# Performance work log

Hardware: AMD Instinct MI355X
Metric: run time of the kernel (lower is better)

## Reference

```python
import jax, jax.numpy as jnp
import numpy as np

N_WIRES = 8
DIM = 1 << N_WIRES  # 256

# --- static precompute: CNOT-ring basis permutation and PauliZ sign matrix ---
# torchquantum convention: wire 0 is the most significant bit of the basis index.
_gates = [(w, w + 1) for w in range(N_WIRES - 1)] + [(N_WIRES - 1, 0)]
_perm = np.empty(DIM, dtype=np.int64)
for b in range(DIM):
    bits = [(b >> (N_WIRES - 1 - w)) & 1 for w in range(N_WIRES)]
    for c, t in _gates:
        if bits[c]:
            bits[t] ^= 1
    _perm[b] = sum(bit << (N_WIRES - 1 - w) for w, bit in enumerate(bits))
_Z = np.array([[1.0 - 2.0 * ((idx >> (N_WIRES - 1 - w)) & 1) for w in range(N_WIRES)]
               for idx in range(DIM)], dtype=np.float32)
# exp_Z[w] = sum_b probs_in[b] * Z[perm[b], w]  (CNOTs permute basis states)
_M = jnp.asarray(_Z[_perm])  # [256, 8]


def _quantum_head(angles):
    """angles: [..., 8] RX angles -> PauliZ expectations [..., 8].

    Circuit: RX(angle_w) on each wire from |0>, CNOT ring, MeasureAll(PauliZ).
    Post-RX state is a product state; CNOTs only permute basis states, so
    probabilities suffice (no complex amplitudes needed).
    """
    half = angles * 0.5
    c2 = jnp.cos(half) ** 2  # P(qubit=0)
    s2 = jnp.sin(half) ** 2  # P(qubit=1)
    # Build the 256-dim joint probability vector via sequential outer products.
    p = jnp.ones(angles.shape[:-1] + (1,), angles.dtype)
    for w in range(N_WIRES):
        pw = jnp.stack([c2[..., w], s2[..., w]], axis=-1)  # [..., 2]
        p = (p[..., :, None] * pw[..., None, :]).reshape(angles.shape[:-1] + (-1,))
    return p @ _M.astype(p.dtype)  # [..., 8]


def setup_inputs() -> dict:
    key = jax.random.key(0)
    ks = jax.random.split(key, 6)
    B, S, E = 8, 512, 768
    scale = 1.0 / np.sqrt(E)
    return {
        "x": jax.random.normal(ks[0], (B, S, E), jnp.float32),
        "W_proj": jax.random.normal(ks[1], (E, E), jnp.float32) * scale,
        "b_proj": jax.random.normal(ks[2], (E,), jnp.float32) * 0.02,
        "theta": jax.random.normal(ks[3], (N_WIRES,), jnp.float32),
        "W_comb": jax.random.normal(ks[4], (E, E), jnp.float32) * scale,
        "b_comb": jax.random.normal(ks[5], (E,), jnp.float32) * 0.02,
    }


def reference(x, W_proj, b_proj, theta, W_comb, b_comb):
    B, S, E = x.shape
    H = E // N_WIRES  # num_heads = 96
    proj = x @ W_proj.T + b_proj                 # [B, S, E] (torch Linear)
    angles = proj.reshape(B, S, H, N_WIRES) + theta  # encoder RX(x) then RX(theta): angles add
    expz = _quantum_head(angles)                 # [B, S, H, 8]
    out = expz.reshape(B, S, E)                  # heads re-concatenated
    # dropout is identity in eval mode
    return out @ W_comb.T + b_comb
```

## Files before the change

kernel.cpp:

```cpp
#include <hip/hip_runtime.h>

typedef _Float16 v8h __attribute__((ext_vector_type(8)));
typedef float    v4f __attribute__((ext_vector_type(4)));

__device__ __forceinline__ void gl_lds16(const void* g, void* l) {
  __builtin_amdgcn_global_load_lds(
      (__attribute__((address_space(1))) void*)(void*)g,
      (__attribute__((address_space(3))) void*)l, 16, 0, 0);
}
__device__ __forceinline__ v8h cvt8(const float4 a, const float4 b) {
  v8h o;
  o[0] = (_Float16)a.x; o[1] = (_Float16)a.y; o[2] = (_Float16)a.z; o[3] = (_Float16)a.w;
  o[4] = (_Float16)b.x; o[5] = (_Float16)b.y; o[6] = (_Float16)b.z; o[7] = (_Float16)b.w;
  return o;
}

__global__ void conv_w(const float4* __restrict__ wp, const float4* __restrict__ wc,
                       v8h* __restrict__ op, v8h* __restrict__ oc) {
  const int n = 73728;
  int i = blockIdx.x * blockDim.x + threadIdx.x;
  const float4* src = (i < n) ? wp : wc;
  v8h* dst = (i < n) ? op : oc;
  const int j = (i < n) ? i : i - n;
  dst[j] = cvt8(src[2 * j], src[2 * j + 1]);
}


__global__ __launch_bounds__(256) void gemm1_qh(
    const float* __restrict__ X,
    const _Float16* __restrict__ B,
    const float* __restrict__ bp,
    const float* __restrict__ theta,
    _Float16* __restrict__ EZ) {
  const int t = threadIdx.x;
  const int b = blockIdx.x;
  const int xcd = b & 7, slot = b >> 3;
  const int bm = xcd * 8 + slot / 12;
  const int bn = slot % 12;

  const int wave = t >> 6, lane = t & 63;
  const int quad = lane >> 4, l16 = lane & 15;
  const int wm = (wave >> 1) * 32, wn = (wave & 1) * 32;

  __shared__ __align__(16) unsigned char smem[32768];
  float* Cs = (float*)smem;

  const float4 th0 = *(const float4*)theta;
  const float4 th1 = *(const float4*)(theta + 4);

  const int r = t >> 3;
  const int cg = t & 7;
  const int lcg = cg ^ (r & 7);

  const float*    Xg = X + (size_t)(bm * 64 + r) * 768 + lcg * 8;
  const _Float16* Bg = B + (size_t)(bn * 64 + r) * 768 + lcg * 8;

  v4f acc[2][2];
#pragma unroll
  for (int i = 0; i < 2; i++)
#pragma unroll
    for (int j = 0; j < 2; j++) acc[i][j] = (v4f){0.f, 0.f, 0.f, 0.f};

  float4 xr[4];
#pragma unroll
  for (int c = 0; c < 2; c++) {
    const float* p = Xg + (size_t)c * 32 * 768;
    xr[2 * c]     = *(const float4*)p;
    xr[2 * c + 1] = *(const float4*)(p + 4);
  }
  {
    _Float16* B0 = (_Float16*)(smem + 16384);
    gl_lds16(Bg, &B0[t * 8]);
    gl_lds16(Bg + (size_t)32 * 768, &B0[2048 + t * 8]);
    _Float16* A0 = (_Float16*)smem;
    *(v8h*)&A0[t * 8]        = cvt8(xr[0], xr[1]);
    *(v8h*)&A0[2048 + t * 8] = cvt8(xr[2], xr[3]);
  }
#pragma unroll
  for (int c = 0; c < 2; c++) {
    const float* p = Xg + (size_t)c * 32 * 768 + 64;
    xr[2 * c]     = *(const float4*)p;
    xr[2 * c + 1] = *(const float4*)(p + 4);
  }
  __syncthreads();

#pragma unroll
  for (int it = 0; it < 12; ++it) {
    _Float16* Ac = (_Float16*)(smem + (it & 1) * 8192);
    _Float16* Bc = (_Float16*)(smem + 16384 + (it & 1) * 8192);
    if (it < 11) {
      _Float16* An = (_Float16*)(smem + ((it + 1) & 1) * 8192);
      _Float16* Bn = (_Float16*)(smem + 16384 + ((it + 1) & 1) * 8192);
      const int kn = (it + 1) * 64;
      gl_lds16(Bg + kn, &Bn[t * 8]);
      gl_lds16(Bg + (size_t)32 * 768 + kn, &Bn[2048 + t * 8]);
      *(v8h*)&An[t * 8]        = cvt8(xr[0], xr[1]);
      *(v8h*)&An[2048 + t * 8] = cvt8(xr[2], xr[3]);
      if (it < 10) {
        const int kf = (it + 2) * 64;
#pragma unroll
        for (int c = 0; c < 2; c++) {
          const float* p = Xg + (size_t)c * 32 * 768 + kf;
          xr[2 * c]     = *(const float4*)p;
          xr[2 * c + 1] = *(const float4*)(p + 4);
        }
      }
    }
#pragma unroll
    for (int q = 0; q < 2; q++) {
      v8h af[2], bf[2];
#pragma unroll
      for (int i = 0; i < 2; i++)
        af[i] = *(const v8h*)&Ac[(wm + i * 16 + l16) * 64 + ((((q << 2) + quad) ^ (l16 & 7)) << 3)];
#pragma unroll
      for (int j = 0; j < 2; j++)
        bf[j] = *(const v8h*)&Bc[(wn + j * 16 + l16) * 64 + ((((q << 2) + quad) ^ (l16 & 7)) << 3)];
#pragma unroll
      for (int i = 0; i < 2; i++)
#pragma unroll
        for (int j = 0; j < 2; j++)
          acc[i][j] = __builtin_amdgcn_mfma_f32_16x16x32_f16(af[i], bf[j], acc[i][j], 0, 0, 0);
    }
    __syncthreads();
  }

  const int r0 = wm + quad * 4;
  const int c0 = wn + l16;
#pragma unroll
  for (int j = 0; j < 2; j++)
#pragma unroll
    for (int i = 0; i < 2; i++)
#pragma unroll
      for (int rr = 0; rr < 4; rr++)
        Cs[(r0 + i * 16 + rr) * 68 + c0 + j * 16] = acc[i][j][rr];
  __syncthreads();

#pragma unroll
  for (int s = 0; s < 2; s++) {
    const int idx = t + s * 256;
    const int row = idx >> 3, h = idx & 7;
    const int gcol = bn * 64 + h * 8;
    const float* cr = &Cs[row * 68 + h * 8];
    const float4 q0 = *(const float4*)cr;
    const float4 q1 = *(const float4*)(cr + 4);
    const float4 b0 = *(const float4*)(bp + gcol);
    const float4 b1 = *(const float4*)(bp + gcol + 4);
    float c[8];
    c[0] = cosf(q0.x + b0.x + th0.x);
    c[1] = cosf(q0.y + b0.y + th0.y);
    c[2] = cosf(q0.z + b0.z + th0.z);
    c[3] = cosf(q0.w + b0.w + th0.w);
    c[4] = cosf(q1.x + b1.x + th1.x);
    c[5] = cosf(q1.y + b1.y + th1.y);
    c[6] = cosf(q1.z + b1.z + th1.z);
    c[7] = cosf(q1.w + b1.w + th1.w);
    float e[8];
    e[0] = c[1] * c[2] * c[3] * c[4] * c[5] * c[6] * c[7];
    float pr = c[0];
#pragma unroll
    for (int w = 1; w < 8; w++) { pr *= c[w]; e[w] = pr; }
    v8h ov;
#pragma unroll
    for (int w = 0; w < 8; w++) ov[w] = (_Float16)e[w];
    *(v8h*)(EZ + (size_t)(bm * 64 + row) * 768 + gcol) = ov;
  }
}

__global__ __launch_bounds__(256) void gemm2(
    const _Float16* __restrict__ A,
    const _Float16* __restrict__ B,
    float* __restrict__ C,
    const float* __restrict__ bias) {
  const int t = threadIdx.x;
  const int b = blockIdx.x;
  const int xcd = b & 7, slot = b >> 3;
  const int bm = xcd * 8 + slot / 12;
  const int bn = slot % 12;

  const int wave = t >> 6, lane = t & 63;
  const int quad = lane >> 4, l16 = lane & 15;
  const int wm = (wave >> 1) * 32, wn = (wave & 1) * 32;

  __shared__ __align__(16) unsigned char smem[32768];

  const int r = t >> 3;
  const int cg = t & 7;
  const int lcg = cg ^ (r & 7);

  const _Float16* Ag = A + (size_t)(bm * 64 + r) * 768 + lcg * 8;
  const _Float16* Bg = B + (size_t)(bn * 64 + r) * 768 + lcg * 8;

  v4f acc[2][2];
#pragma unroll
  for (int i = 0; i < 2; i++)
#pragma unroll
    for (int j = 0; j < 2; j++) acc[i][j] = (v4f){0.f, 0.f, 0.f, 0.f};

  {
    _Float16* A0 = (_Float16*)smem;
    _Float16* B0 = (_Float16*)(smem + 16384);
    gl_lds16(Ag, &A0[t * 8]);
    gl_lds16(Ag + (size_t)32 * 768, &A0[2048 + t * 8]);
    gl_lds16(Bg, &B0[t * 8]);
    gl_lds16(Bg + (size_t)32 * 768, &B0[2048 + t * 8]);
  }
  __syncthreads();

#pragma unroll
  for (int it = 0; it < 12; ++it) {
    _Float16* Ac = (_Float16*)(smem + (it & 1) * 8192);
    _Float16* Bc = (_Float16*)(smem + 16384 + (it & 1) * 8192);
    if (it < 11) {
      _Float16* An = (_Float16*)(smem + ((it + 1) & 1) * 8192);
      _Float16* Bn = (_Float16*)(smem + 16384 + ((it + 1) & 1) * 8192);
      const int kn = (it + 1) * 64;
      gl_lds16(Ag + kn, &An[t * 8]);
      gl_lds16(Ag + (size_t)32 * 768 + kn, &An[2048 + t * 8]);
      gl_lds16(Bg + kn, &Bn[t * 8]);
      gl_lds16(Bg + (size_t)32 * 768 + kn, &Bn[2048 + t * 8]);
    }
#pragma unroll
    for (int q = 0; q < 2; q++) {
      v8h af[2], bf[2];
#pragma unroll
      for (int i = 0; i < 2; i++)
        af[i] = *(const v8h*)&Ac[(wm + i * 16 + l16) * 64 + ((((q << 2) + quad) ^ (l16 & 7)) << 3)];
#pragma unroll
      for (int j = 0; j < 2; j++)
        bf[j] = *(const v8h*)&Bc[(wn + j * 16 + l16) * 64 + ((((q << 2) + quad) ^ (l16 & 7)) << 3)];
#pragma unroll
      for (int ii = 0; ii < 2; ii++)
#pragma unroll
        for (int j = 0; j < 2; j++)
          acc[ii][j] = __builtin_amdgcn_mfma_f32_16x16x32_f16(af[ii], bf[j], acc[ii][j], 0, 0, 0);
    }
    __syncthreads();
  }

  const int row0 = bm * 64 + wm + quad * 4;
  const int col0 = bn * 64 + wn + l16;
#pragma unroll
  for (int j = 0; j < 2; j++) {
    const int col = col0 + j * 16;
    const float bv = bias[col];
#pragma unroll
    for (int i = 0; i < 2; i++) {
#pragma unroll
      for (int rr = 0; rr < 4; rr++) {
        C[(size_t)(row0 + i * 16 + rr) * 768 + col] = acc[i][j][rr] + bv;
      }
    }
  }
}

extern "C" void kernel_launch(void* const* d_in, const int* in_sizes, int n_in,
                              void* d_out, int out_size, void* d_ws, size_t ws_size,
                              hipStream_t stream) {
  const float* x     = (const float*)d_in[0];
  const float* Wp    = (const float*)d_in[1];
  const float* bp    = (const float*)d_in[2];
  const float* theta = (const float*)d_in[3];
  const float* Wcf   = (const float*)d_in[4];
  const float* bc    = (const float*)d_in[5];
  float* out = (float*)d_out;

  const size_t EE = (size_t)768 * 768;

  _Float16* WPH = (_Float16*)d_ws;
  _Float16* WCH = WPH + EE;
  _Float16* EZ  = WCH + EE;

  conv_w<<<(int)(2 * EE / 8 / 256), 256, 0, stream>>>(
      (const float4*)Wp, (const float4*)Wcf, (v8h*)WPH, (v8h*)WCH);

  gemm1_qh<<<768, 256, 0, stream>>>(x, WPH, bp, theta, EZ);

  gemm2<<<768, 256, 0, stream>>>(EZ, WCH, out, bc);
}
```

Baseline: 99.33 us.

## Fuse weight conversion and both GEMMs into one persistent kernel with row flags

Drops the separate weight-conversion kernel and converts fp32 weights to fp16 inline while staging tiles, and merges the two GEMM kernels into one launch. Blocks that share a row tile synchronize through a global atomic counter before running the second GEMM on the EZ rows their siblings produced. This removes two kernel launches and the intermediate fp16 weight buffers. In exchange, every block converts weight tiles redundantly and spins on flags, which relies on all 768 blocks being co-resident (hence launch_bounds with 3 blocks per CU) to avoid deadlock. It also adds a memset launch.

New measurement: 207.1 us. 2.08x slower.

```diff
diff --git a/kernel.cpp b/kernel.cpp
--- a/kernel.cpp
+++ b/kernel.cpp
@@ -15,23 +15,16 @@
   return o;
 }
 
-__global__ void conv_w(const float4* __restrict__ wp, const float4* __restrict__ wc,
-                       v8h* __restrict__ op, v8h* __restrict__ oc) {
-  const int n = 73728;
-  int i = blockIdx.x * blockDim.x + threadIdx.x;
-  const float4* src = (i < n) ? wp : wc;
-  v8h* dst = (i < n) ? op : oc;
-  const int j = (i < n) ? i : i - n;
-  dst[j] = cvt8(src[2 * j], src[2 * j + 1]);
-}
-
-
-__global__ __launch_bounds__(256) void gemm1_qh(
+__global__ __launch_bounds__(256, 3) void fused_all(
     const float* __restrict__ X,
-    const _Float16* __restrict__ B,
+    const float* __restrict__ Wp,
     const float* __restrict__ bp,
     const float* __restrict__ theta,
-    _Float16* __restrict__ EZ) {
+    const float* __restrict__ Wc,
+    const float* __restrict__ bc,
+    float* __restrict__ OUT,
+    _Float16* __restrict__ EZ,
+    int* __restrict__ flags) {
   const int t = threadIdx.x;
   const int b = blockIdx.x;
   const int xcd = b & 7, slot = b >> 3;
@@ -52,202 +45,216 @@
   const int cg = t & 7;
   const int lcg = cg ^ (r & 7);
 
-  const float*    Xg = X + (size_t)(bm * 64 + r) * 768 + lcg * 8;
-  const _Float16* Bg = B + (size_t)(bn * 64 + r) * 768 + lcg * 8;
-
   v4f acc[2][2];
-#pragma unroll
-  for (int i = 0; i < 2; i++)
-#pragma unroll
-    for (int j = 0; j < 2; j++) acc[i][j] = (v4f){0.f, 0.f, 0.f, 0.f};
-
-  float4 xr[4];
-#pragma unroll
-  for (int c = 0; c < 2; c++) {
-    const float* p = Xg + (size_t)c * 32 * 768;
-    xr[2 * c]     = *(const float4*)p;
-    xr[2 * c + 1] = *(const float4*)(p + 4);
+
+  {
+    const float* Xg = X  + (size_t)(bm * 64 + r) * 768 + lcg * 8;
+    const float* Bg = Wp + (size_t)(bn * 64 + r) * 768 + lcg * 8;
+
+#pragma unroll
+    for (int i = 0; i < 2; i++)
+#pragma unroll
+      for (int j = 0; j < 2; j++) acc[i][j] = (v4f){0.f, 0.f, 0.f, 0.f};
+
+    float4 xr[4], br[4];
+#pragma unroll
+    for (int c = 0; c < 2; c++) {
+      const float* px = Xg + (size_t)c * 32 * 768;
+      const float* pb = Bg + (size_t)c * 32 * 768;
+      xr[2 * c] = *(const float4*)px; xr[2 * c + 1] = *(const float4*)(px + 4);
+      br[2 * c] = *(const float4*)pb; br[2 * c + 1] = *(const float4*)(pb + 4);
+    }
+    {
+      _Float16* A0 = (_Float16*)smem;
+      _Float16* B0 = (_Float16*)(smem + 16384);
+      *(v8h*)&A0[t * 8]        = cvt8(xr[0], xr[1]);
+      *(v8h*)&A0[2048 + t * 8] = cvt8(xr[2], xr[3]);
+      *(v8h*)&B0[t * 8]        = cvt8(br[0], br[1]);
+      *(v8h*)&B0[2048 + t * 8] = cvt8(br[2], br[3]);
+    }
+#pragma unroll
+    for (int c = 0; c < 2; c++) {
+      const float* px = Xg + (size_t)c * 32 * 768 + 64;
+      const float* pb = Bg + (size_t)c * 32 * 768 + 64;
+      xr[2 * c] = *(const float4*)px; xr[2 * c + 1] = *(const float4*)(px + 4);
+      br[2 * c] = *(const float4*)pb; br[2 * c + 1] = *(const float4*)(pb + 4);
+    }
+    __syncthreads();
+
+#pragma unroll
+    for (int it = 0; it < 12; ++it) {
+      _Float16* Ac = (_Float16*)(smem + (it & 1) * 8192);
+      _Float16* Bc = (_Float16*)(smem + 16384 + (it & 1) * 8192);
+      if (it < 11) {
+        _Float16* An = (_Float16*)(smem + ((it + 1) & 1) * 8192);
+        _Float16* Bn = (_Float16*)(smem + 16384 + ((it + 1) & 1) * 8192);
+        *(v8h*)&An[t * 8]        = cvt8(xr[0], xr[1]);
+        *(v8h*)&An[2048 + t * 8] = cvt8(xr[2], xr[3]);
+        *(v8h*)&Bn[t * 8]        = cvt8(br[0], br[1]);
+        *(v8h*)&Bn[2048 + t * 8] = cvt8(br[2], br[3]);
+        if (it < 10) {
+          const int kf = (it + 2) * 64;
+#pragma unroll
+          for (int c = 0; c < 2; c++) {
+            const float* px = Xg + (size_t)c * 32 * 768 + kf;
+            const float* pb = Bg + (size_t)c * 32 * 768 + kf;
+            xr[2 * c] = *(const float4*)px; xr[2 * c + 1] = *(const float4*)(px + 4);
+            br[2 * c] = *(const float4*)pb; br[2 * c + 1] = *(const float4*)(pb + 4);
+          }
+        }
+      }
+#pragma unroll
+      for (int q = 0; q < 2; q++) {
+        v8h af[2], bf[2];
+#pragma unroll
+        for (int i = 0; i < 2; i++)
+          af[i] = *(const v8h*)&Ac[(wm + i * 16 + l16) * 64 + ((((q << 2) + quad) ^ (l16 & 7)) << 3)];
+#pragma unroll
+        for (int j = 0; j < 2; j++)
+          bf[j] = *(const v8h*)&Bc[(wn + j * 16 + l16) * 64 + ((((q << 2) + quad) ^ (l16 & 7)) << 3)];
+#pragma unroll
+        for (int i = 0; i < 2; i++)
+#pragma unroll
+          for (int j = 0; j < 2; j++)
+            acc[i][j] = __builtin_amdgcn_mfma_f32_16x16x32_f16(af[i], bf[j], acc[i][j], 0, 0, 0);
+      }
+      __syncthreads();
+    }
+
+    const int r0 = wm + quad * 4;
+    const int c0 = wn + l16;
+#pragma unroll
+    for (int j = 0; j < 2; j++)
+#pragma unroll
+      for (int i = 0; i < 2; i++)
+#pragma unroll
+        for (int rr = 0; rr < 4; rr++)
+          Cs[(r0 + i * 16 + rr) * 68 + c0 + j * 16] = acc[i][j][rr];
+    __syncthreads();
+
+#pragma unroll
+    for (int s = 0; s < 2; s++) {
+      const int idx = t + s * 256;
+      const int row = idx >> 3, h = idx & 7;
+      const int gcol = bn * 64 + h * 8;
+      const float* cr = &Cs[row * 68 + h * 8];
+      const float4 q0 = *(const float4*)cr;
+      const float4 q1 = *(const float4*)(cr + 4);
+      const float4 b0 = *(const float4*)(bp + gcol);
+      const float4 b1 = *(const float4*)(bp + gcol + 4);
+      float c[8];
+      c[0] = cosf(q0.x + b0.x + th0.x);
+      c[1] = cosf(q0.y + b0.y + th0.y);
+      c[2] = cosf(q0.z + b0.z + th0.z);
+      c[3] = cosf(q0.w + b0.w + th0.w);
+      c[4] = cosf(q1.x + b1.x + th1.x);
+      c[5] = cosf(q1.y + b1.y + th1.y);
+      c[6] = cosf(q1.z + b1.z + th1.z);
+      c[7] = cosf(q1.w + b1.w + th1.w);
+      float e[8];
+      e[0] = c[1] * c[2] * c[3] * c[4] * c[5] * c[6] * c[7];
+      float pr = c[0];
+#pragma unroll
+      for (int w = 1; w < 8; w++) { pr *= c[w]; e[w] = pr; }
+      v8h ov;
+#pragma unroll
+      for (int w = 0; w < 8; w++) ov[w] = (_Float16)e[w];
+      *(v8h*)(EZ + (size_t)(bm * 64 + row) * 768 + gcol) = ov;
+    }
   }
-  {
-    _Float16* B0 = (_Float16*)(smem + 16384);
-    gl_lds16(Bg, &B0[t * 8]);
-    gl_lds16(Bg + (size_t)32 * 768, &B0[2048 + t * 8]);
-    _Float16* A0 = (_Float16*)smem;
-    *(v8h*)&A0[t * 8]        = cvt8(xr[0], xr[1]);
-    *(v8h*)&A0[2048 + t * 8] = cvt8(xr[2], xr[3]);
-  }
-#pragma unroll
-  for (int c = 0; c < 2; c++) {
-    const float* p = Xg + (size_t)c * 32 * 768 + 64;
-    xr[2 * c]     = *(const float4*)p;
-    xr[2 * c + 1] = *(const float4*)(p + 4);
+
+  __threadfence();
+  __syncthreads();
+  if (t == 0)
+    __hip_atomic_fetch_add(&flags[bm], 1, __ATOMIC_RELEASE, __HIP_MEMORY_SCOPE_AGENT);
+
+  if (t == 0) {
+    while (__hip_atomic_load(&flags[bm], __ATOMIC_ACQUIRE, __HIP_MEMORY_SCOPE_AGENT) < 12)
+      __builtin_amdgcn_s_sleep(8);
   }
   __syncthreads();
 
-#pragma unroll
-  for (int it = 0; it < 12; ++it) {
-    _Float16* Ac = (_Float16*)(smem + (it & 1) * 8192);
-    _Float16* Bc = (_Float16*)(smem + 16384 + (it & 1) * 8192);
-    if (it < 11) {
-      _Float16* An = (_Float16*)(smem + ((it + 1) & 1) * 8192);
-      _Float16* Bn = (_Float16*)(smem + 16384 + ((it + 1) & 1) * 8192);
-      const int kn = (it + 1) * 64;
-      gl_lds16(Bg + kn, &Bn[t * 8]);
-      gl_lds16(Bg + (size_t)32 * 768 + kn, &Bn[2048 + t * 8]);
-      *(v8h*)&An[t * 8]        = cvt8(xr[0], xr[1]);
-      *(v8h*)&An[2048 + t * 8] = cvt8(xr[2], xr[3]);
-      if (it < 10) {
-        const int kf = (it + 2) * 64;
-#pragma unroll
-        for (int c = 0; c < 2; c++) {
-          const float* p = Xg + (size_t)c * 32 * 768 + kf;
-          xr[2 * c]     = *(const float4*)p;
-          xr[2 * c + 1] = *(const float4*)(p + 4);
+  {
+    const _Float16* Ag = EZ + (size_t)(bm * 64 + r) * 768 + lcg * 8;
+    const float*    Bg = Wc + (size_t)(bn * 64 + r) * 768 + lcg * 8;
+
+#pragma unroll
+    for (int i = 0; i < 2; i++)
+#pragma unroll
+      for (int j = 0; j < 2; j++) acc[i][j] = (v4f){0.f, 0.f, 0.f, 0.f};
+
+    float4 wr[4];
+    {
+      _Float16* A0 = (_Float16*)smem;
+      _Float16* B0 = (_Float16*)(smem + 16384);
+      gl_lds16(Ag, &A0[t * 8]);
+      gl_lds16(Ag + (size_t)32 * 768, &A0[2048 + t * 8]);
+#pragma unroll
+      for (int c = 0; c < 2; c++) {
+        const float* pb = Bg + (size_t)c * 32 * 768;
+        wr[2 * c] = *(const float4*)pb; wr[2 * c + 1] = *(const float4*)(pb + 4);
+      }
+      *(v8h*)&B0[t * 8]        = cvt8(wr[0], wr[1]);
+      *(v8h*)&B0[2048 + t * 8] = cvt8(wr[2], wr[3]);
+    }
+#pragma unroll
+    for (int c = 0; c < 2; c++) {
+      const float* pb = Bg + (size_t)c * 32 * 768 + 64;
+      wr[2 * c] = *(const float4*)pb; wr[2 * c + 1] = *(const float4*)(pb + 4);
+    }
+    __syncthreads();
+
+#pragma unroll
+    for (int it = 0; it < 12; ++it) {
+      _Float16* Ac = (_Float16*)(smem + (it & 1) * 8192);
+      _Float16* Bc = (_Float16*)(smem + 16384 + (it & 1) * 8192);
+      if (it < 11) {
+        _Float16* An = (_Float16*)(smem + ((it + 1) & 1) * 8192);
+        _Float16* Bn = (_Float16*)(smem + 16384 + ((it + 1) & 1) * 8192);
+        const int kn = (it + 1) * 64;
+        gl_lds16(Ag + kn, &An[t * 8]);
+        gl_lds16(Ag + (size_t)32 * 768 + kn, &An[2048 + t * 8]);
+        *(v8h*)&Bn[t * 8]        = cvt8(wr[0], wr[1]);
+        *(v8h*)&Bn[2048 + t * 8] = cvt8(wr[2], wr[3]);
+        if (it < 10) {
+          const int kf = (it + 2) * 64;
+#pragma unroll
+          for (int c = 0; c < 2; c++) {
+            const float* pb = Bg + (size_t)c * 32 * 768 + kf;
+            wr[2 * c] = *(const float4*)pb; wr[2 * c + 1] = *(const float4*)(pb + 4);
+          }
         }
       }
-    }
-#pragma unroll
-    for (int q = 0; q < 2; q++) {
-      v8h af[2], bf[2];
-#pragma unroll
-      for (int i = 0; i < 2; i++)
-        af[i] = *(const v8h*)&Ac[(wm + i * 16 + l16) * 64 + ((((q << 2) + quad) ^ (l16 & 7)) << 3)];
-#pragma unroll
-      for (int j = 0; j < 2; j++)
-        bf[j] = *(const v8h*)&Bc[(wn + j * 16 + l16) * 64 + ((((q << 2) + quad) ^ (l16 & 7)) << 3)];
-#pragma unroll
-      for (int i = 0; i < 2; i++)
+#pragma unroll
+      for (int q = 0; q < 2; q++) {
+        v8h af[2], bf[2];
+#pragma unroll
+        for (int i = 0; i < 2; i++)
+          af[i] = *(const v8h*)&Ac[(wm + i * 16 + l16) * 64 + ((((q << 2) + quad) ^ (l16 & 7)) << 3)];
 #pragma unroll
         for (int j = 0; j < 2; j++)
-          acc[i][j] = __builtin_amdgcn_mfma_f32_16x16x32_f16(af[i], bf[j], acc[i][j], 0, 0, 0);
-    }
-    __syncthreads();
-  }
-
-  const int r0 = wm + quad * 4;
-  const int c0 = wn + l16;
-#pragma unroll
-  for (int j = 0; j < 2; j++)
-#pragma unroll
-    for (int i = 0; i < 2; i++)
-#pragma unroll
-      for (int rr = 0; rr < 4; rr++)
-        Cs[(r0 + i * 16 + rr) * 68 + c0 + j * 16] = acc[i][j][rr];
-  __syncthreads();
-
-#pragma unroll
-  for (int s = 0; s < 2; s++) {
-    const int idx = t + s * 256;
-    const int row = idx >> 3, h = idx & 7;
-    const int gcol = bn * 64 + h * 8;
-    const float* cr = &Cs[row * 68 + h * 8];
-    const float4 q0 = *(const float4*)cr;
-    const float4 q1 = *(const float4*)(cr + 4);
-    const float4 b0 = *(const float4*)(bp + gcol);
-    const float4 b1 = *(const float4*)(bp + gcol + 4);
-    float c[8];
-    c[0] = cosf(q0.x + b0.x + th0.x);
-    c[1] = cosf(q0.y + b0.y + th0.y);
-    c[2] = cosf(q0.z + b0.z + th0.z);
-    c[3] = cosf(q0.w + b0.w + th0.w);
-    c[4] = cosf(q1.x + b1.x + th1.x);
-    c[5] = cosf(q1.y + b1.y + th1.y);
-    c[6] = cosf(q1.z + b1.z + th1.z);
-    c[7] = cosf(q1.w + b1.w + th1.w);
-    float e[8];
-    e[0] = c[1] * c[2] * c[3] * c[4] * c[5] * c[6] * c[7];
-    float pr = c[0];
-#pragma unroll
-    for (int w = 1; w < 8; w++) { pr *= c[w]; e[w] = pr; }
-    v8h ov;
-#pragma unroll
-    for (int w = 0; w < 8; w++) ov[w] = (_Float16)e[w];
-    *(v8h*)(EZ + (size_t)(bm * 64 + row) * 768 + gcol) = ov;
-  }
-}
-
-__global__ __launch_bounds__(256) void gemm2(
-    const _Float16* __restrict__ A,
-    const _Float16* __restrict__ B,
-    float* __restrict__ C,
-    const float* __restrict__ bias) {
-  const int t = threadIdx.x;
-  const int b = blockIdx.x;
-  const int xcd = b & 7, slot = b >> 3;
-  const int bm = xcd * 8 + slot / 12;
-  const int bn = slot % 12;
-
-  const int wave = t >> 6, lane = t & 63;
-  const int quad = lane >> 4, l16 = lane & 15;
-  const int wm = (wave >> 1) * 32, wn = (wave & 1) * 32;
-
-  __shared__ __align__(16) unsigned char smem[32768];
-
-  const int r = t >> 3;
-  const int cg = t & 7;
-  const int lcg = cg ^ (r & 7);
-
-  const _Float16* Ag = A + (size_t)(bm * 64 + r) * 768 + lcg * 8;
-  const _Float16* Bg = B + (size_t)(bn * 64 + r) * 768 + lcg * 8;
-
-  v4f acc[2][2];
-#pragma unroll
-  for (int i = 0; i < 2; i++)
-#pragma unroll
-    for (int j = 0; j < 2; j++) acc[i][j] = (v4f){0.f, 0.f, 0.f, 0.f};
-
-  {
-    _Float16* A0 = (_Float16*)smem;
-    _Float16* B0 = (_Float16*)(smem + 16384);
-    gl_lds16(Ag, &A0[t * 8]);
-    gl_lds16(Ag + (size_t)32 * 768, &A0[2048 + t * 8]);
-    gl_lds16(Bg, &B0[t * 8]);
-    gl_lds16(Bg + (size_t)32 * 768, &B0[2048 + t * 8]);
-  }
-  __syncthreads();
-
-#pragma unroll
-  for (int it = 0; it < 12; ++it) {
-    _Float16* Ac = (_Float16*)(smem + (it & 1) * 8192);
-    _Float16* Bc = (_Float16*)(smem + 16384 + (it & 1) * 8192);
-    if (it < 11) {
-      _Float16* An = (_Float16*)(smem + ((it + 1) & 1) * 8192);
-      _Float16* Bn = (_Float16*)(smem + 16384 + ((it + 1) & 1) * 8192);
-      const int kn = (it + 1) * 64;
-      gl_lds16(Ag + kn, &An[t * 8]);
-      gl_lds16(Ag + (size_t)32 * 768 + kn, &An[2048 + t * 8]);
-      gl_lds16(Bg + kn, &Bn[t * 8]);
-      gl_lds16(Bg + (size_t)32 * 768 + kn, &Bn[2048 + t * 8]);
-    }
-#pragma unroll
-    for (int q = 0; q < 2; q++) {
-      v8h af[2], bf[2];
-#pragma unroll
-      for (int i = 0; i < 2; i++)
-        af[i] = *(const v8h*)&Ac[(wm + i * 16 + l16) * 64 + ((((q << 2) + quad) ^ (l16 & 7)) << 3)];
-#pragma unroll
-      for (int j = 0; j < 2; j++)
-        bf[j] = *(const v8h*)&Bc[(wn + j * 16 + l16) * 64 + ((((q << 2) + quad) ^ (l16 & 7)) << 3)];
-#pragma unroll
-      for (int ii = 0; ii < 2; ii++)
-#pragma unroll
-        for (int j = 0; j < 2; j++)
-          acc[ii][j] = __builtin_amdgcn_mfma_f32_16x16x32_f16(af[ii], bf[j], acc[ii][j], 0, 0, 0);
-    }
-    __syncthreads();
-  }
-
-  const int row0 = bm * 64 + wm + quad * 4;
-  const int col0 = bn * 64 + wn + l16;
-#pragma unroll
-  for (int j = 0; j < 2; j++) {
-    const int col = col0 + j * 16;
-    const float bv = bias[col];
-#pragma unroll
-    for (int i = 0; i < 2; i++) {
-#pragma unroll
-      for (int rr = 0; rr < 4; rr++) {
-        C[(size_t)(row0 + i * 16 + rr) * 768 + col] = acc[i][j][rr] + bv;
+          bf[j] = *(const v8h*)&Bc[(wn + j * 16 + l16) * 64 + ((((q << 2) + quad) ^ (l16 & 7)) << 3)];
+#pragma unroll
+        for (int ii = 0; ii < 2; ii++)
+#pragma unroll
+          for (int j = 0; j < 2; j++)
+            acc[ii][j] = __builtin_amdgcn_mfma_f32_16x16x32_f16(af[ii], bf[j], acc[ii][j], 0, 0, 0);
+      }
+      __syncthreads();
+    }
+
+    const int row0 = bm * 64 + wm + quad * 4;
+    const int col0 = bn * 64 + wn + l16;
+#pragma unroll
+    for (int j = 0; j < 2; j++) {
+      const int col = col0 + j * 16;
+      const float bv = bc[col];
+#pragma unroll
+      for (int i = 0; i < 2; i++) {
+#pragma unroll
+        for (int rr = 0; rr < 4; rr++) {
+          OUT[(size_t)(row0 + i * 16 + rr) * 768 + col] = acc[i][j][rr] + bv;
+        }
       }
     }
   }
@@ -264,16 +271,9 @@
   const float* bc    = (const float*)d_in[5];
   float* out = (float*)d_out;
 
-  const size_t EE = (size_t)768 * 768;
-
-  _Float16* WPH = (_Float16*)d_ws;
-  _Float16* WCH = WPH + EE;
-  _Float16* EZ  = WCH + EE;
-
-  conv_w<<<(int)(2 * EE / 8 / 256), 256, 0, stream>>>(
-      (const float4*)Wp, (const float4*)Wcf, (v8h*)WPH, (v8h*)WCH);
-
-  gemm1_qh<<<768, 256, 0, stream>>>(x, WPH, bp, theta, EZ);
-
-  gemm2<<<768, 256, 0, stream>>>(EZ, WCH, out, bc);
-}
+  _Float16* EZ = (_Float16*)d_ws;
+  int* flags = (int*)((char*)d_ws + (size_t)4096 * 768 * 2);
+
+  hipMemsetAsync(flags, 0, 64 * sizeof(int), stream);
+  fused_all<<<768, 256, 0, stream>>>(x, Wp, bp, theta, Wcf, bc, out, EZ, flags);
+}
```
